# Kernel tuning notes

Hardware: AMD Instinct MI355X
Metric: run time of the kernel (lower is better)

The kernel has to match this reference:

```python
import jax, jax.numpy as jnp
import numpy as np

B, D, H = 8192, 1024, 1024


def setup_inputs() -> dict:
    key = jax.random.key(0)
    k = jax.random.split(key, 6)
    s_x = 1.0 / np.sqrt(D)
    s_h = 1.0 / np.sqrt(H)
    return {
        "x": jax.random.normal(k[0], (B, D), dtype=jnp.float32),
        "h_prev": jax.random.normal(k[1], (B, H), dtype=jnp.float32),
        "c_prev": jax.random.normal(k[2], (B, H), dtype=jnp.float32),
        # Stacked gate weights in order [i, f, o, g] (exactly equivalent to
        # the 8 separate nn.Linear layers, fused into 2 GEMMs).
        "Wx": jax.random.uniform(k[3], (4 * H, D), jnp.float32, -s_x, s_x),
        "Wh": jax.random.uniform(k[4], (4 * H, H), jnp.float32, -s_h, s_h),
        # combined bias of W_* and U_* linears per gate
        "b": jax.random.uniform(k[5], (4 * H,), jnp.float32, -s_x, s_x),
    }


def reference(x, h_prev, c_prev, Wx, Wh, b):
    # gates: [B, 4H], gate order i, f, o, g
    gates = x @ Wx.T + h_prev @ Wh.T + b
    i, f, o, g = jnp.split(gates, 4, axis=-1)
    c_t = jax.nn.sigmoid(f) * c_prev + jax.nn.sigmoid(i) * jnp.tanh(g)
    h_t = jax.nn.sigmoid(o) * jnp.tanh(c_t)
    return (h_t, c_t)
```

## Files before the change

### kernel.cpp

```cpp
#include <hip/hip_runtime.h>
#include <hip/hip_bf16.h>
#include <stdint.h>

#define B_ROWS 8192
#define D_DIM  1024
#define H_DIM  1024
#define K_DIM  2048
#define N_GATES 4096

#define BM 128
#define BN 64
#define BK 64

#define KC (K_DIM / 32)
#define A_M16 (B_ROWS / 16)
#define W_N16 (N_GATES / 16)
#define A_CHUNKS (A_M16 * KC)
#define W_CHUNKS (W_N16 * KC)
#define A_WS_BYTES ((size_t)A_CHUNKS * 1024)
#define W_WS_BYTES ((size_t)W_CHUNKS * 1024)

#define TBM 256
#define TBH 64
#define NT  KC
#define NBUF 4
#define SBUF (16 * 512)

typedef __bf16 bf16x8 __attribute__((ext_vector_type(8)));
typedef float  f32x4  __attribute__((ext_vector_type(4)));
typedef int    i32x4  __attribute__((ext_vector_type(4)));
using bf16_t = __hip_bfloat16;

__device__ __forceinline__ float sigm(float x) {
  return 1.0f / (1.0f + __expf(-x));
}
__device__ __forceinline__ float tanh_fast(float x) {
  return 1.0f - 2.0f / (__expf(2.0f * x) + 1.0f);
}

__device__ __forceinline__ void async_ld16(const void* g, void* l) {
  __builtin_amdgcn_global_load_lds(
      (const __attribute__((address_space(1))) unsigned int*)g,
      (__attribute__((address_space(3))) unsigned int*)l, 16, 0, 0);
}

#define FENCE() asm volatile("" ::: "memory")
#define BAR() do { FENCE(); __builtin_amdgcn_s_barrier(); FENCE(); } while (0)

__global__ __launch_bounds__(256) void pack_tiles(
    const float* __restrict__ x, const float* __restrict__ h,
    const float* __restrict__ Wx, const float* __restrict__ Wh,
    bf16_t* __restrict__ aws, bf16_t* __restrict__ wws) {
  const int wave = threadIdx.x >> 6, lane = threadIdx.x & 63;
  const int row = lane >> 2;
  const int kq  = lane & 3;
  const int LT4 = (((lane & 15) << 2) | (lane >> 4)) << 2;
  const int c0 = (blockIdx.x * 4 + wave) * 4;

#pragma unroll
  for (int cc = 0; cc < 4; ++cc) {
    int c = c0 + cc;
    const float* src;
    size_t soff;
    bf16_t* dst;
    if (c < A_CHUNKS) {
      const int m16 = c / KC, k32 = c % KC;
      const int k = k32 * 32 + kq * 8;
      src = (k < D_DIM) ? x : h;
      soff = (size_t)(m16 * 16 + row) * 1024 + (k & 1023);
      dst = aws + (size_t)c * 512;
    } else {
      const int cw = c - A_CHUNKS;
      const int n16 = cw / KC, k32 = cw % KC;
      const int k = k32 * 32 + kq * 8;
      src = (k < D_DIM) ? Wx : Wh;
      soff = (size_t)(n16 * 16 + row) * 1024 + (k & 1023);
      dst = wws + (size_t)cw * 512;
    }
    const f32x4 a = *(const f32x4*)(src + soff);
    const f32x4 b = *(const f32x4*)(src + soff + 4);
    bf16x8 v;
#pragma unroll
    for (int i = 0; i < 4; ++i) { v[i] = (__bf16)a[i]; v[i + 4] = (__bf16)b[i]; }
    const i32x4 w = __builtin_bit_cast(i32x4, v);
    i32x4 p;
    p[0] = __builtin_amdgcn_ds_bpermute(LT4, w[0]);
    p[1] = __builtin_amdgcn_ds_bpermute(LT4, w[1]);
    p[2] = __builtin_amdgcn_ds_bpermute(LT4, w[2]);
    p[3] = __builtin_amdgcn_ds_bpermute(LT4, w[3]);
    *(i32x4*)(dst + lane * 8) = p;
  }
}

__global__ __launch_bounds__(512, 2) void lstm_mfma(
    const bf16_t* __restrict__ aws, const bf16_t* __restrict__ wws,
    const float* __restrict__ c_prev, const float* __restrict__ bias,
    float* __restrict__ h_out, float* __restrict__ c_out) {
  __shared__ __align__(16) bf16_t sA[NBUF * SBUF];
  __shared__ __align__(16) bf16_t sB[NBUF * SBUF];

  const int tid  = threadIdx.x;
  const int wave = tid >> 6;
  const int lane = tid & 63;

  const int xcd = blockIdx.x & 7;
  const int idx = blockIdx.x >> 3;
  const int m_blk = (xcd >> 1) * 8 + (idx & 7);
  const int n_blk = (xcd & 1) * 8 + (idx >> 3);
  const int m0 = m_blk * TBM;
  const int n0 = n_blk * TBH;
  const int m16_0 = m0 >> 4;
  const int n16_0 = n0 >> 4;

  const int wm = wave >> 2;
  const int wh = wave & 3;
  const int lr = lane & 15, quad = lane >> 4;

  f32x4 acc[4][8];
#pragma unroll
  for (int g = 0; g < 4; ++g)
#pragma unroll
    for (int mi = 0; mi < 8; ++mi) {
      f32x4 z = {0.0f, 0.0f, 0.0f, 0.0f};
      acc[g][mi] = z;
    }

  const bf16_t* gA  = aws + (size_t)(m16_0 + wave) * KC * 512 + lane * 8;
  const bf16_t* gA8 = gA + (size_t)8 * KC * 512;
  const int n16w = (wave >> 2) * (H_DIM / 16) + n16_0 + (wave & 3);
  const bf16_t* gB  = wws + (size_t)n16w * KC * 512 + lane * 8;
  const bf16_t* gB8 = gB + (size_t)128 * KC * 512;
  bf16_t* lA  = sA + wave * 512 + lane * 8;
  bf16_t* lA8 = lA + 8 * 512;
  bf16_t* lB  = sB + wave * 512 + lane * 8;
  bf16_t* lB8 = lB + 8 * 512;

  auto STAGE_A = [&](int tt) {
    const int bo = (tt & 3) * SBUF;
    const size_t go = (size_t)tt * 512;
    async_ld16(gA + go, lA + bo);
    async_ld16(gA8 + go, lA8 + bo);
  };
  auto STAGE_B = [&](int tt) {
    const int bo = (tt & 3) * SBUF;
    const size_t go = (size_t)tt * 512;
    async_ld16(gB + go, lB + bo);
    async_ld16(gB8 + go, lB8 + bo);
  };

  const int rA = wm * 8 * 512 + lane * 8;
  const int rB = wh * 512 + lane * 8;

  auto LD_AF = [&](bf16x8 (&dst)[4], int bufo, int half4) {
#pragma unroll
    for (int x = 0; x < 4; ++x)
      dst[x] = *(const bf16x8*)&sA[bufo + rA + (half4 + x) * 512];
  };
  auto LD_BW = [&](bf16x8 (&dst)[4], int bufo) {
#pragma unroll
    for (int g = 0; g < 4; ++g)
      dst[g] = *(const bf16x8*)&sB[bufo + rB + g * 4 * 512];
  };
  auto MMA = [&](const bf16x8 (&a)[4], const bf16x8 (&b)[4], int s) {
    __builtin_amdgcn_s_setprio(1);
#pragma unroll
    for (int g = 0; g < 4; ++g)
#pragma unroll
      for (int x = 0; x < 4; ++x)
        acc[g][s + x] = __builtin_amdgcn_mfma_f32_16x16x32_bf16(
            a[x], b[g], acc[g][s + x], 0, 0, 0);
    __builtin_amdgcn_s_setprio(0);
  };

  STAGE_A(0); STAGE_B(0); STAGE_A(1); STAGE_B(1); STAGE_A(2); STAGE_B(2);
  asm volatile("s_waitcnt vmcnt(8)" ::: "memory");
  BAR();

  bf16x8 afA[4], bwA[4], afB[4], bwB[4];
  LD_AF(afA, 0, 0);
  LD_BW(bwA, 0);

  auto tile_step = [&](int t, bf16x8 (&afc)[4], bf16x8 (&bwc)[4],
                       bf16x8 (&afn)[4], bf16x8 (&bwn)[4]) {
    const int cbo = (t & 3) * SBUF;
    const int nbo = ((t + 1) & 3) * SBUF;
    bf16x8 af2[4];
    LD_AF(af2, cbo, 4);
    if (t + 3 < NT) STAGE_A(t + 3);
    MMA(afc, bwc, 0);
    if (t + 3 < NT)      asm volatile("s_waitcnt vmcnt(6)" ::: "memory");
    else if (t + 2 < NT) asm volatile("s_waitcnt vmcnt(4)" ::: "memory");
    else if (t + 1 < NT) asm volatile("s_waitcnt vmcnt(0)" ::: "memory");
    BAR();
    if (t + 1 < NT) { LD_AF(afn, nbo, 0); LD_BW(bwn, nbo); }
    if (t + 3 < NT) STAGE_B(t + 3);
    MMA(af2, bwc, 4);
    BAR();
  };

  for (int t = 0; t < NT; t += 2) {
    tile_step(t,     afA, bwA, afB, bwB);
    tile_step(t + 1, afB, bwB, afA, bwA);
  }

  const int col = n0 + wh * 16 + lr;
  const float bi  = bias[col];
  const float bfv = bias[H_DIM + col];
  const float bo  = bias[2 * H_DIM + col];
  const float bg  = bias[3 * H_DIM + col];
#pragma unroll
  for (int mi = 0; mi < 8; ++mi) {
#pragma unroll
    for (int r = 0; r < 4; ++r) {
      const int m = m0 + wm * 128 + mi * 16 + quad * 4 + r;
      const size_t off = (size_t)m * H_DIM + col;
      const float iv = acc[0][mi][r] + bi;
      const float fv = acc[1][mi][r] + bfv;
      const float ov = acc[2][mi][r] + bo;
      const float gv = acc[3][mi][r] + bg;
      const float cp = c_prev[off];
      const float ct = sigm(fv) * cp + sigm(iv) * tanh_fast(gv);
      h_out[off] = sigm(ov) * tanh_fast(ct);
      c_out[off] = ct;
    }
  }
}

__device__ __forceinline__ int sw_(int row, int chunk) {
  return row * BK + ((chunk ^ (row & 7)) << 3);
}

__global__ __launch_bounds__(256, 2) void lstm_f32(
    const float* __restrict__ x, const float* __restrict__ h_prev,
    const float* __restrict__ c_prev, const float* __restrict__ Wx,
    const float* __restrict__ Wh, const float* __restrict__ bias,
    float* __restrict__ h_out, float* __restrict__ c_out) {
  __shared__ bf16_t sA[BM * BK];
  __shared__ bf16_t sB[4 * BN * BK];
  const int tid = threadIdx.x, wave = tid >> 6, lane = tid & 63;
  const int m0 = blockIdx.x * BM, n0 = blockIdx.y * BN;
  const int wm = wave >> 1, wn = wave & 1;
  const int lr = lane & 15, quad = lane >> 4;
  f32x4 acc[4][4][2];
#pragma unroll
  for (int g = 0; g < 4; ++g)
#pragma unroll
    for (int ti = 0; ti < 4; ++ti)
#pragma unroll
      for (int tj = 0; tj < 2; ++tj) {
        f32x4 z = {0.0f, 0.0f, 0.0f, 0.0f};
        acc[g][ti][tj] = z;
      }
  const int srow = lane >> 3, lc = lane & 7, scol = lc << 3;
  for (int k0 = 0; k0 < K_DIM; k0 += BK) {
    const float* aSrc; const float* wSrc; int kh;
    if (k0 < D_DIM) { aSrc = x; wSrc = Wx; kh = k0; }
    else            { aSrc = h_prev; wSrc = Wh; kh = k0 - D_DIM; }
    f32x4 stg[12][2];
#pragma unroll
    for (int t = 0; t < 12; ++t) {
      const int chunk = wave + t * 4;
      const float* g;
      if (chunk < 16) {
        g = aSrc + (size_t)(m0 + chunk * 8 + srow) * 1024 + kh + scol;
      } else {
        const int j = chunk - 16;
        g = wSrc + (size_t)((j >> 3) * H_DIM + n0 + (j & 7) * 8 + srow) * 1024 + kh + scol;
      }
      stg[t][0] = *(const f32x4*)g;
      stg[t][1] = *(const f32x4*)(g + 4);
    }
    __syncthreads();
#pragma unroll
    for (int t = 0; t < 12; ++t) {
      const int chunk = wave + t * 4;
      bf16x8 v;
#pragma unroll
      for (int i = 0; i < 4; ++i) {
        v[i] = (__bf16)stg[t][0][i];
        v[i + 4] = (__bf16)stg[t][1][i];
      }
      bf16_t* dst;
      if (chunk < 16) dst = &sA[sw_(chunk * 8 + srow, lc)];
      else {
        const int j = chunk - 16;
        dst = &sB[(j >> 3) * (BN * BK) + sw_((j & 7) * 8 + srow, lc)];
      }
      *(bf16x8*)dst = v;
    }
    __syncthreads();
#pragma unroll
    for (int kk = 0; kk < BK; kk += 32) {
      const int cbase = kk >> 3;
      bf16x8 af[4];
#pragma unroll
      for (int ti = 0; ti < 4; ++ti)
        af[ti] = *(const bf16x8*)&sA[sw_(wm * 64 + ti * 16 + lr, cbase + quad)];
      bf16x8 bw[4][2];
#pragma unroll
      for (int g = 0; g < 4; ++g)
#pragma unroll
        for (int tj = 0; tj < 2; ++tj)
          bw[g][tj] = *(const bf16x8*)
              &sB[g * (BN * BK) + sw_(wn * 32 + tj * 16 + lr, cbase + quad)];
#pragma unroll
      for (int g = 0; g < 4; ++g)
#pragma unroll
        for (int ti = 0; ti < 4; ++ti)
#pragma unroll
          for (int tj = 0; tj < 2; ++tj)
            acc[g][ti][tj] = __builtin_amdgcn_mfma_f32_16x16x32_bf16(
                af[ti], bw[g][tj], acc[g][ti][tj], 0, 0, 0);
    }
  }
#pragma unroll
  for (int tj = 0; tj < 2; ++tj) {
    const int n = n0 + wn * 32 + tj * 16 + lr;
    const float bi = bias[n], bf = bias[H_DIM + n];
    const float bo = bias[2 * H_DIM + n], bg = bias[3 * H_DIM + n];
#pragma unroll
    for (int ti = 0; ti < 4; ++ti)
#pragma unroll
      for (int r = 0; r < 4; ++r) {
        const int m = m0 + wm * 64 + ti * 16 + quad * 4 + r;
        const size_t off = (size_t)m * H_DIM + n;
        const float iv = acc[0][ti][tj][r] + bi;
        const float fv = acc[1][ti][tj][r] + bf;
        const float ov = acc[2][ti][tj][r] + bo;
        const float gv = acc[3][ti][tj][r] + bg;
        const float cp = c_prev[off];
        const float ct = sigm(fv) * cp + sigm(iv) * tanh_fast(gv);
        h_out[off] = sigm(ov) * tanh_fast(ct);
        c_out[off] = ct;
      }
  }
}

extern "C" void kernel_launch(void* const* d_in, const int* in_sizes, int n_in,
                              void* d_out, int out_size, void* d_ws, size_t ws_size,
                              hipStream_t stream) {
  const float* x      = (const float*)d_in[0];
  const float* h_prev = (const float*)d_in[1];
  const float* c_prev = (const float*)d_in[2];
  const float* Wx     = (const float*)d_in[3];
  const float* Wh     = (const float*)d_in[4];
  const float* b      = (const float*)d_in[5];
  float* h_out = (float*)d_out;
  float* c_out = (float*)d_out + (size_t)B_ROWS * H_DIM;

  if (ws_size >= A_WS_BYTES + W_WS_BYTES) {
    bf16_t* aws = (bf16_t*)d_ws;
    bf16_t* wws = (bf16_t*)((char*)d_ws + A_WS_BYTES);
    pack_tiles<<<(A_CHUNKS + W_CHUNKS) / 16, 256, 0, stream>>>(x, h_prev, Wx,
                                                               Wh, aws, wws);
    const int nblk = (B_ROWS / TBM) * (H_DIM / TBH);
    lstm_mfma<<<nblk, 512, 0, stream>>>(aws, wws, c_prev, b, h_out, c_out);
  } else {
    dim3 grid(B_ROWS / BM, H_DIM / BN, 1);
    lstm_f32<<<grid, 256, 0, stream>>>(x, h_prev, c_prev, Wx, Wh, b, h_out, c_out);
  }
}
```

Measured before the change: 300.2 us.

## Halve MFMA block tile to 128 rows with triple-buffered single-barrier pipeline

Shrinks the per-block M tile from 256 to 128 rows and halves per-wave accumulators. This allows four blocks per CU instead of two, and the grid mapping is changed to cover twice as many M blocks. The four-buffer, double-register-set pipeline with two barriers per K step becomes a simpler three-buffer loop with one barrier per step. The goal is more occupancy and less register pressure and sync overhead, at the cost of lower arithmetic intensity per block and more global/LDS traffic for the weight tiles.

```diff
diff --git a/kernel.cpp b/kernel.cpp
--- a/kernel.cpp
+++ b/kernel.cpp
@@ -20,11 +20,11 @@
 #define A_WS_BYTES ((size_t)A_CHUNKS * 1024)
 #define W_WS_BYTES ((size_t)W_CHUNKS * 1024)
 
-#define TBM 256
+#define TBM 128
 #define TBH 64
 #define NT  KC
-#define NBUF 4
-#define SBUF (16 * 512)
+#define SA_BUF (8 * 512)
+#define SB_BUF (16 * 512)
 
 typedef __bf16 bf16x8 __attribute__((ext_vector_type(8)));
 typedef float  f32x4  __attribute__((ext_vector_type(4)));
@@ -92,12 +92,12 @@
   }
 }
 
-__global__ __launch_bounds__(512, 2) void lstm_mfma(
+__global__ __launch_bounds__(512, 4) void lstm_mfma(
     const bf16_t* __restrict__ aws, const bf16_t* __restrict__ wws,
     const float* __restrict__ c_prev, const float* __restrict__ bias,
     float* __restrict__ h_out, float* __restrict__ c_out) {
-  __shared__ __align__(16) bf16_t sA[NBUF * SBUF];
-  __shared__ __align__(16) bf16_t sB[NBUF * SBUF];
+  __shared__ __align__(16) bf16_t sA[3 * SA_BUF];
+  __shared__ __align__(16) bf16_t sB[3 * SB_BUF];
 
   const int tid  = threadIdx.x;
   const int wave = tid >> 6;
@@ -105,8 +105,8 @@
 
   const int xcd = blockIdx.x & 7;
   const int idx = blockIdx.x >> 3;
-  const int m_blk = (xcd >> 1) * 8 + (idx & 7);
-  const int n_blk = (xcd & 1) * 8 + (idx >> 3);
+  const int m_blk = (xcd >> 1) * 16 + (idx & 15);
+  const int n_blk = (xcd & 1) * 8 + (idx >> 4);
   const int m0 = m_blk * TBM;
   const int n0 = n_blk * TBH;
   const int m16_0 = m0 >> 4;
@@ -116,91 +116,61 @@
   const int wh = wave & 3;
   const int lr = lane & 15, quad = lane >> 4;
 
-  f32x4 acc[4][8];
+  f32x4 acc[4][4];
 #pragma unroll
   for (int g = 0; g < 4; ++g)
 #pragma unroll
-    for (int mi = 0; mi < 8; ++mi) {
+    for (int mi = 0; mi < 4; ++mi) {
       f32x4 z = {0.0f, 0.0f, 0.0f, 0.0f};
       acc[g][mi] = z;
     }
 
-  const bf16_t* gA  = aws + (size_t)(m16_0 + wave) * KC * 512 + lane * 8;
-  const bf16_t* gA8 = gA + (size_t)8 * KC * 512;
+  const bf16_t* gA = aws + (size_t)(m16_0 + wave) * KC * 512 + lane * 8;
   const int n16w = (wave >> 2) * (H_DIM / 16) + n16_0 + (wave & 3);
   const bf16_t* gB  = wws + (size_t)n16w * KC * 512 + lane * 8;
   const bf16_t* gB8 = gB + (size_t)128 * KC * 512;
   bf16_t* lA  = sA + wave * 512 + lane * 8;
-  bf16_t* lA8 = lA + 8 * 512;
   bf16_t* lB  = sB + wave * 512 + lane * 8;
   bf16_t* lB8 = lB + 8 * 512;
 
-  auto STAGE_A = [&](int tt) {
-    const int bo = (tt & 3) * SBUF;
+  auto STAGE = [&](int tt) {
+    const int b3 = tt % 3;
     const size_t go = (size_t)tt * 512;
-    async_ld16(gA + go, lA + bo);
-    async_ld16(gA8 + go, lA8 + bo);
+    async_ld16(gA + go, lA + b3 * SA_BUF);
+    async_ld16(gB + go, lB + b3 * SB_BUF);
+    async_ld16(gB8 + go, lB8 + b3 * SB_BUF);
   };
-  auto STAGE_B = [&](int tt) {
-    const int bo = (tt & 3) * SBUF;
-    const size_t go = (size_t)tt * 512;
-    async_ld16(gB + go, lB + bo);
-    async_ld16(gB8 + go, lB8 + bo);
-  };
-
-  const int rA = wm * 8 * 512 + lane * 8;
+
+  const int rA = wm * 4 * 512 + lane * 8;
   const int rB = wh * 512 + lane * 8;
 
-  auto LD_AF = [&](bf16x8 (&dst)[4], int bufo, int half4) {
+  STAGE(0); STAGE(1);
+  asm volatile("s_waitcnt vmcnt(3)" ::: "memory");
+  BAR();
+
+#pragma unroll 1
+  for (int t = 0; t < NT; ++t) {
+    const int aoff = (t % 3) * SA_BUF;
+    const int boff = (t % 3) * SB_BUF;
+    bf16x8 af[4], bw[4];
 #pragma unroll
     for (int x = 0; x < 4; ++x)
-      dst[x] = *(const bf16x8*)&sA[bufo + rA + (half4 + x) * 512];
-  };
-  auto LD_BW = [&](bf16x8 (&dst)[4], int bufo) {
+      af[x] = *(const bf16x8*)&sA[aoff + rA + x * 512];
 #pragma unroll
     for (int g = 0; g < 4; ++g)
-      dst[g] = *(const bf16x8*)&sB[bufo + rB + g * 4 * 512];
-  };
-  auto MMA = [&](const bf16x8 (&a)[4], const bf16x8 (&b)[4], int s) {
+      bw[g] = *(const bf16x8*)&sB[boff + rB + g * 2048];
+    if (t + 2 < NT) STAGE(t + 2);
     __builtin_amdgcn_s_setprio(1);
 #pragma unroll
     for (int g = 0; g < 4; ++g)
 #pragma unroll
       for (int x = 0; x < 4; ++x)
-        acc[g][s + x] = __builtin_amdgcn_mfma_f32_16x16x32_bf16(
-            a[x], b[g], acc[g][s + x], 0, 0, 0);
+        acc[g][x] = __builtin_amdgcn_mfma_f32_16x16x32_bf16(
+            af[x], bw[g], acc[g][x], 0, 0, 0);
     __builtin_amdgcn_s_setprio(0);
-  };
-
-  STAGE_A(0); STAGE_B(0); STAGE_A(1); STAGE_B(1); STAGE_A(2); STAGE_B(2);
-  asm volatile("s_waitcnt vmcnt(8)" ::: "memory");
-  BAR();
-
-  bf16x8 afA[4], bwA[4], afB[4], bwB[4];
-  LD_AF(afA, 0, 0);
-  LD_BW(bwA, 0);
-
-  auto tile_step = [&](int t, bf16x8 (&afc)[4], bf16x8 (&bwc)[4],
-                       bf16x8 (&afn)[4], bf16x8 (&bwn)[4]) {
-    const int cbo = (t & 3) * SBUF;
-    const int nbo = ((t + 1) & 3) * SBUF;
-    bf16x8 af2[4];
-    LD_AF(af2, cbo, 4);
-    if (t + 3 < NT) STAGE_A(t + 3);
-    MMA(afc, bwc, 0);
-    if (t + 3 < NT)      asm volatile("s_waitcnt vmcnt(6)" ::: "memory");
-    else if (t + 2 < NT) asm volatile("s_waitcnt vmcnt(4)" ::: "memory");
+    if (t + 2 < NT)      asm volatile("s_waitcnt vmcnt(3)" ::: "memory");
     else if (t + 1 < NT) asm volatile("s_waitcnt vmcnt(0)" ::: "memory");
     BAR();
-    if (t + 1 < NT) { LD_AF(afn, nbo, 0); LD_BW(bwn, nbo); }
-    if (t + 3 < NT) STAGE_B(t + 3);
-    MMA(af2, bwc, 4);
-    BAR();
-  };
-
-  for (int t = 0; t < NT; t += 2) {
-    tile_step(t,     afA, bwA, afB, bwB);
-    tile_step(t + 1, afB, bwB, afA, bwA);
   }
 
   const int col = n0 + wh * 16 + lr;
@@ -209,10 +179,10 @@
   const float bo  = bias[2 * H_DIM + col];
   const float bg  = bias[3 * H_DIM + col];
 #pragma unroll
-  for (int mi = 0; mi < 8; ++mi) {
+  for (int mi = 0; mi < 4; ++mi) {
 #pragma unroll
     for (int r = 0; r < 4; ++r) {
-      const int m = m0 + wm * 128 + mi * 16 + quad * 4 + r;
+      const int m = m0 + wm * 64 + mi * 16 + quad * 4 + r;
       const size_t off = (size_t)m * H_DIM + col;
       const float iv = acc[0][mi][r] + bi;
       const float fv = acc[1][mi][r] + bfv;
```

After: 300.6 us. Within noise of the previous version (+0.1%).
